# Kernel tuning notes

Measured on AMD Instinct MI355X. Metric: run time of the kernel, lower is better.

Reference implementation:

```python
import jax, jax.numpy as jnp
import numpy as np

E, B, S, D, R = 8, 8, 2048, 512, 128
MAX_MAG = 0.1  # config.geometric.max_rotation_magnitude


def _plane_indices(dim, r):
    # Row-major enumeration of (i, j), i < j, truncated to first r planes,
    # matching the nested loop in create_rotation_matrix.
    pairs = []
    for i in range(dim):
        for j in range(i + 1, dim):
            pairs.append((i, j))
            if len(pairs) == r:
                return np.asarray(pairs, np.int32)
    return np.asarray(pairs, np.int32)


def setup_inputs() -> dict:
    key = jax.random.key(0)
    k1, k2, k3 = jax.random.split(key, 3)
    x = jax.random.normal(k1, (B, S, D), dtype=jnp.float32)
    theta = jax.random.normal(k2, (E, R), dtype=jnp.float32) * 0.1
    # projector init: 0.1 * orthogonal + I  (per torch init in __init__)
    Wr = jax.random.normal(k3, (E, D, D), dtype=jnp.float32)
    Q, _ = jnp.linalg.qr(Wr)
    proj_w = 0.1 * Q + jnp.eye(D, dtype=jnp.float32)
    return {"x": x, "theta": theta, "proj_w": proj_w}


def _rotation_matrix(theta_e, ij):
    # Sequential right-multiplication by Givens rotations.
    # M <- M @ G(i,j,a) only touches columns i and j:
    #   col_i' =  c*col_i + s*col_j ;  col_j' = -s*col_i + c*col_j
    angles = jnp.tanh(theta_e) * MAX_MAG  # [R]

    def step(M, inp):
        i, j, a = inp
        c, s = jnp.cos(a), jnp.sin(a)
        ci = M[:, i]
        cj = M[:, j]
        M = M.at[:, i].set(c * ci + s * cj)
        M = M.at[:, j].set(-s * ci + c * cj)
        return M, None

    M0 = jnp.eye(D, dtype=theta_e.dtype)
    M, _ = jax.lax.scan(step, M0, (ij[:, 0], ij[:, 1], angles))
    return M


def reference(x, theta, proj_w):
    ij = jnp.asarray(_plane_indices(D, R))  # [R, 2] static plane indices
    Rm = jax.vmap(lambda t: _rotation_matrix(t, ij))(theta)  # [E, D, D]
    # rotated = flat_x @ R^T per expert
    rotated = jnp.einsum('bsd,ekd->ebsk', x, Rm)            # [E, B, S, D]
    # projector: Linear(bias=False) -> y = rotated @ W^T
    out = jnp.einsum('ebsk,eok->ebso', rotated, proj_w)     # [E, B, S, D]
    return out
```

## Files before the change

### kernel.cpp

```cpp
#include <hip/hip_runtime.h>
#include <hip/hip_bf16.h>

#define E_ 8
#define B_ 8
#define S_ 2048
#define D_ 512
#define R_ 128
#define M_TOT (B_ * S_)

typedef __attribute__((ext_vector_type(8))) short bf16x8;
typedef __attribute__((ext_vector_type(4))) float f32x4;

__device__ __forceinline__ void gload_lds16(void* lds, const void* g) {
  __builtin_amdgcn_global_load_lds(
      (const __attribute__((address_space(1))) void*)g,
      (__attribute__((address_space(3))) void*)lds, 16, 0, 0);
}

#define ROT_B 16
#define WT_B 2048
#define CX_B 4096
__global__ __launch_bounds__(256) void prep_fused(
    const float* __restrict__ x, const float* __restrict__ theta,
    const float* __restrict__ pw, __hip_bfloat16* __restrict__ xb,
    __hip_bfloat16* __restrict__ Wb) {
  int blk = blockIdx.x;
  int t = threadIdx.x;
  if (blk < ROT_B) {
    __shared__ float cs[R_], ss[R_];
    __shared__ float Pch[256][17];
    __shared__ __hip_bfloat16 Wch[256][18];
    int e = blk >> 1;
    int r0 = (blk & 1) * 256;
    if (t < R_) {
      float a = tanhf(theta[e * R_ + t]) * 0.1f;
      cs[t] = cosf(a);
      ss[t] = sinf(a);
    }
    const float* Pe = pw + (size_t)e * D_ * D_;
    __hip_bfloat16* We = Wb + (size_t)e * D_ * D_;
    float u = Pe[(size_t)(r0 + t) * D_];
    __syncthreads();
    for (int c = 0; c < 8; ++c) {
      for (int i = t; i < 256 * 16; i += 256) {
        int row = i >> 4, col = i & 15;
        Pch[row][col] = Pe[(size_t)(r0 + row) * D_ + 1 + 16 * c + col];
      }
      __syncthreads();
#pragma unroll
      for (int kk = 0; kk < 16; ++kk) {
        int k = 16 * c + kk;
        float pj = Pch[t][kk];
        Wch[t][kk] = __float2bfloat16(cs[k] * pj - ss[k] * u);
        u = cs[k] * u + ss[k] * pj;
      }
      __syncthreads();
      for (int i = t; i < 256 * 16; i += 256) {
        int row = i >> 4, col = i & 15;
        We[(size_t)(r0 + row) * D_ + 1 + 16 * c + col] = Wch[row][col];
      }
      __syncthreads();
    }
    We[(size_t)(r0 + t) * D_] = __float2bfloat16(u);
  } else if (blk < ROT_B + WT_B) {
    int g = (blk - ROT_B) * 256 + t;
    int gidx = g & 127;
    if (gidx < 32) return;
    float4 v = ((const float4*)pw)[g];
    union { short4 s; __hip_bfloat16 h[4]; } u;
    u.h[0] = __float2bfloat16(v.x);
    u.h[1] = __float2bfloat16(v.y);
    u.h[2] = __float2bfloat16(v.z);
    u.h[3] = __float2bfloat16(v.w);
    if (gidx > 32) {
      ((short4*)Wb)[g] = u.s;
    } else {
      Wb[(size_t)g * 4 + 1] = u.h[1];
      Wb[(size_t)g * 4 + 2] = u.h[2];
      Wb[(size_t)g * 4 + 3] = u.h[3];
    }
  } else {
    int i = (blk - ROT_B - WT_B) * 256 + t;
#pragma unroll
    for (int rep = 0; rep < 2; ++rep) {
      int idx = i + rep * (CX_B * 256);
      float4 v = ((const float4*)x)[idx];
      union { short4 s; __hip_bfloat16 h[4]; } u;
      u.h[0] = __float2bfloat16(v.x);
      u.h[1] = __float2bfloat16(v.y);
      u.h[2] = __float2bfloat16(v.z);
      u.h[3] = __float2bfloat16(v.w);
      ((short4*)xb)[idx] = u.s;
    }
  }
}

__global__ __launch_bounds__(512, 2) void gemm_xw(
    const __hip_bfloat16* __restrict__ Xb,
    const __hip_bfloat16* __restrict__ Wb,
    float* __restrict__ out)
{
  constexpr int BK = 64;
  constexpr int KD = D_, ND = D_;
  constexpr int NT = KD / BK;
  __shared__ __align__(16) __hip_bfloat16 As[4][128 * 64];
  __shared__ __align__(16) __hip_bfloat16 Bs[4][128 * 64];

  int bx = blockIdx.x;
  int swz = (bx & 7) * 128 + (bx >> 3);
  int mt = swz >> 4;
  int e  = (swz >> 1) & 7;
  int nt = swz & 1;

  int tid = threadIdx.x;
  int wave = tid >> 6, lane = tid & 63;
  int lr = lane & 15, lk = lane >> 4;
  int wm = wave >> 2, wn = wave & 3;

  const __hip_bfloat16* Ag = Xb + (size_t)(mt * 256) * KD;
  const __hip_bfloat16* Bg = Wb + ((size_t)e * ND + (size_t)nt * 256) * KD;

  int srow = lane >> 3;
  int scol = ((lane & 7) ^ srow) * 8;

  int axor0 = ((0 * 4 + lk) ^ (lr & 7)) * 8;
  int axor1 = ((1 * 4 + lk) ^ (lr & 7)) * 8;

  f32x4 acc[8][4];
#pragma unroll
  for (int i = 0; i < 8; ++i)
#pragma unroll
    for (int j = 0; j < 4; ++j) acc[i][j] = (f32x4){0.f, 0.f, 0.f, 0.f};

#define STAGE(ARR, GBASE, h, tt)                                             \
  {                                                                          \
    int slot_ = (2 * (tt) + (h)) & 3;                                        \
    _Pragma("unroll") for (int g = 0; g < 2; ++g) {                          \
      gload_lds16(&ARR[slot_][(wave * 16 + g * 8) * 64],                     \
                  (GBASE) + (size_t)((h) * 128 + wave * 16 + g * 8 + srow) * \
                                KD + (tt) * BK + scol);                      \
    }                                                                        \
  }

#define QUAD(mh, nh)                                                         \
  {                                                                          \
    __builtin_amdgcn_s_setprio(1);                                           \
    _Pragma("unroll") for (int m4 = 0; m4 < 4; ++m4)                         \
        _Pragma("unroll") for (int n2 = 0; n2 < 2; ++n2)                     \
            _Pragma("unroll") for (int kk = 0; kk < 2; ++kk)                 \
                acc[(mh)*4 + m4][(nh)*2 + n2] =                              \
                    __builtin_amdgcn_mfma_f32_16x16x32_bf16(                 \
                        af[(mh)*4 + m4][kk], bfr[(nh)*2 + n2][kk],           \
                        acc[(mh)*4 + m4][(nh)*2 + n2], 0, 0, 0);             \
    __builtin_amdgcn_s_setprio(0);                                           \
  }

  STAGE(As, Ag, 0, 0); STAGE(As, Ag, 1, 0);
  STAGE(Bs, Bg, 0, 0); STAGE(Bs, Bg, 1, 0);
  STAGE(As, Ag, 0, 1); STAGE(As, Ag, 1, 1);
  STAGE(Bs, Bg, 0, 1);

#pragma unroll
  for (int t = 0; t < NT; ++t) {
    if (t < NT - 1) {
      asm volatile("s_waitcnt vmcnt(6)" ::: "memory");
    } else {
      asm volatile("s_waitcnt vmcnt(0)" ::: "memory");
    }
    __builtin_amdgcn_s_barrier();
    asm volatile("" ::: "memory");

    const __hip_bfloat16* Asl = As[(2 * t + wm) & 3];
    const __hip_bfloat16* Bsl = Bs[(2 * t + (wn >> 1)) & 3];
    bf16x8 af[8][2], bfr[4][2];
#pragma unroll
    for (int mi = 0; mi < 8; ++mi) {
      int rb = (mi * 16 + lr) * 64;
      af[mi][0] = *(const bf16x8*)&Asl[rb + axor0];
      af[mi][1] = *(const bf16x8*)&Asl[rb + axor1];
    }
#pragma unroll
    for (int ni = 0; ni < 4; ++ni) {
      int rb = ((wn & 1) * 64 + ni * 16 + lr) * 64;
      bfr[ni][0] = *(const bf16x8*)&Bsl[rb + axor0];
      bfr[ni][1] = *(const bf16x8*)&Bsl[rb + axor1];
    }
    if (t + 1 < NT) STAGE(Bs, Bg, 1, t + 1);
    __syncthreads();
    QUAD(0, 0);

    if (t + 2 < NT) STAGE(As, Ag, 0, t + 2);
    asm volatile("" ::: "memory");
    __builtin_amdgcn_s_barrier();
    asm volatile("" ::: "memory");
    QUAD(0, 1);

    if (t + 2 < NT) STAGE(As, Ag, 1, t + 2);
    asm volatile("" ::: "memory");
    __builtin_amdgcn_s_barrier();
    asm volatile("" ::: "memory");
    QUAD(1, 0);

    if (t + 2 < NT) STAGE(Bs, Bg, 0, t + 2);
    asm volatile("" ::: "memory");
    __builtin_amdgcn_s_barrier();
    asm volatile("" ::: "memory");
    QUAD(1, 1);
  }
#undef STAGE
#undef QUAD

  size_t obase = (size_t)e * M_TOT * ND;
  int row0 = mt * 256 + wm * 128;
  int col0 = nt * 256 + wn * 64;
#pragma unroll
  for (int mi = 0; mi < 8; ++mi)
#pragma unroll
    for (int ni = 0; ni < 4; ++ni) {
      int r0 = row0 + mi * 16 + lk * 4;
      int c = col0 + ni * 16 + lr;
      float* op = out + obase + (size_t)r0 * ND + c;
#pragma unroll
      for (int q = 0; q < 4; ++q) op[(size_t)q * ND] = acc[mi][ni][q];
    }
}

extern "C" void kernel_launch(void* const* d_in, const int* in_sizes, int n_in,
                              void* d_out, int out_size, void* d_ws, size_t ws_size,
                              hipStream_t stream) {
  const float* x = (const float*)d_in[0];
  const float* theta = (const float*)d_in[1];
  const float* proj_w = (const float*)d_in[2];
  float* out = (float*)d_out;

  __hip_bfloat16* xb = (__hip_bfloat16*)d_ws;
  __hip_bfloat16* Wb = (__hip_bfloat16*)((char*)d_ws +
                        (size_t)M_TOT * D_ * sizeof(__hip_bfloat16));

  hipLaunchKernelGGL(prep_fused, dim3(ROT_B + WT_B + CX_B), dim3(256), 0,
                     stream, x, theta, proj_w, xb, Wb);
  hipLaunchKernelGGL(gemm_xw, dim3(E_ * (M_TOT / 256) * (D_ / 256)), dim3(512),
                     0, stream, xb, Wb, out);
}
```

Before: 128.1 us.

## Split LDS fragment loads into phases interleaved with MFMA quadrants

The GEMM main loop now loads A and B fragments from shared memory in halves, just before the MFMA quadrant that needs them, instead of loading all fragments up front. Explicit lgkmcnt waits and sched barriers enforce the order. The global-to-LDS prefetch order is also rearranged so slots are refilled only after every wave has finished reading them. The aim is to overlap LDS reads with matrix work and to lower peak fragment register pressure. The cost is extra barriers and waits, which could serialize the waves.

```diff
diff --git a/kernel.cpp b/kernel.cpp
--- a/kernel.cpp
+++ b/kernel.cpp
@@ -142,7 +142,7 @@
     }                                                                        \
   }
 
-#define QUAD(mh, nh)                                                         \
+#define QUAD(AF, BF, mh, nh)                                                 \
   {                                                                          \
     __builtin_amdgcn_s_setprio(1);                                           \
     _Pragma("unroll") for (int m4 = 0; m4 < 4; ++m4)                         \
@@ -150,15 +150,19 @@
             _Pragma("unroll") for (int kk = 0; kk < 2; ++kk)                 \
                 acc[(mh)*4 + m4][(nh)*2 + n2] =                              \
                     __builtin_amdgcn_mfma_f32_16x16x32_bf16(                 \
-                        af[(mh)*4 + m4][kk], bfr[(nh)*2 + n2][kk],           \
+                        AF[m4][kk], BF[n2][kk],                              \
                         acc[(mh)*4 + m4][(nh)*2 + n2], 0, 0, 0);             \
     __builtin_amdgcn_s_setprio(0);                                           \
   }
 
+#define LGKM0                                                                \
+  asm volatile("s_waitcnt lgkmcnt(0)" ::: "memory");                         \
+  __builtin_amdgcn_sched_barrier(0);
+
   STAGE(As, Ag, 0, 0); STAGE(As, Ag, 1, 0);
   STAGE(Bs, Bg, 0, 0); STAGE(Bs, Bg, 1, 0);
+  STAGE(Bs, Bg, 0, 1);
   STAGE(As, Ag, 0, 1); STAGE(As, Ag, 1, 1);
-  STAGE(Bs, Bg, 0, 1);
 
 #pragma unroll
   for (int t = 0; t < NT; ++t) {
@@ -168,47 +172,58 @@
       asm volatile("s_waitcnt vmcnt(0)" ::: "memory");
     }
     __builtin_amdgcn_s_barrier();
-    asm volatile("" ::: "memory");
 
     const __hip_bfloat16* Asl = As[(2 * t + wm) & 3];
     const __hip_bfloat16* Bsl = Bs[(2 * t + (wn >> 1)) & 3];
-    bf16x8 af[8][2], bfr[4][2];
-#pragma unroll
-    for (int mi = 0; mi < 8; ++mi) {
+
+    bf16x8 af_lo[4][2], bfr_lo[2][2];
+#pragma unroll
+    for (int mi = 0; mi < 4; ++mi) {
       int rb = (mi * 16 + lr) * 64;
-      af[mi][0] = *(const bf16x8*)&Asl[rb + axor0];
-      af[mi][1] = *(const bf16x8*)&Asl[rb + axor1];
-    }
-#pragma unroll
-    for (int ni = 0; ni < 4; ++ni) {
+      af_lo[mi][0] = *(const bf16x8*)&Asl[rb + axor0];
+      af_lo[mi][1] = *(const bf16x8*)&Asl[rb + axor1];
+    }
+#pragma unroll
+    for (int ni = 0; ni < 2; ++ni) {
       int rb = ((wn & 1) * 64 + ni * 16 + lr) * 64;
-      bfr[ni][0] = *(const bf16x8*)&Bsl[rb + axor0];
-      bfr[ni][1] = *(const bf16x8*)&Bsl[rb + axor1];
+      bfr_lo[ni][0] = *(const bf16x8*)&Bsl[rb + axor0];
+      bfr_lo[ni][1] = *(const bf16x8*)&Bsl[rb + axor1];
     }
     if (t + 1 < NT) STAGE(Bs, Bg, 1, t + 1);
-    __syncthreads();
-    QUAD(0, 0);
-
-    if (t + 2 < NT) STAGE(As, Ag, 0, t + 2);
-    asm volatile("" ::: "memory");
-    __builtin_amdgcn_s_barrier();
-    asm volatile("" ::: "memory");
-    QUAD(0, 1);
-
-    if (t + 2 < NT) STAGE(As, Ag, 1, t + 2);
-    asm volatile("" ::: "memory");
-    __builtin_amdgcn_s_barrier();
-    asm volatile("" ::: "memory");
-    QUAD(1, 0);
-
+    LGKM0;
+    __builtin_amdgcn_s_barrier();
+    QUAD(af_lo, bfr_lo, 0, 0);
+
+    bf16x8 bfr_hi[2][2];
+#pragma unroll
+    for (int ni = 0; ni < 2; ++ni) {
+      int rb = ((wn & 1) * 64 + (2 + ni) * 16 + lr) * 64;
+      bfr_hi[ni][0] = *(const bf16x8*)&Bsl[rb + axor0];
+      bfr_hi[ni][1] = *(const bf16x8*)&Bsl[rb + axor1];
+    }
+    LGKM0;
+    __builtin_amdgcn_s_barrier();
+    QUAD(af_lo, bfr_hi, 0, 1);
+
+    bf16x8 af_hi[4][2];
+#pragma unroll
+    for (int mi = 0; mi < 4; ++mi) {
+      int rb = ((4 + mi) * 16 + lr) * 64;
+      af_hi[mi][0] = *(const bf16x8*)&Asl[rb + axor0];
+      af_hi[mi][1] = *(const bf16x8*)&Asl[rb + axor1];
+    }
     if (t + 2 < NT) STAGE(Bs, Bg, 0, t + 2);
-    asm volatile("" ::: "memory");
-    __builtin_amdgcn_s_barrier();
-    asm volatile("" ::: "memory");
-    QUAD(1, 1);
+    LGKM0;
+    __builtin_amdgcn_s_barrier();
+    QUAD(af_hi, bfr_lo, 1, 0);
+
+    if (t + 2 < NT) { STAGE(As, Ag, 0, t + 2); STAGE(As, Ag, 1, t + 2); }
+    __builtin_amdgcn_s_barrier();
+    QUAD(af_hi, bfr_hi, 1, 1);
   }
 #undef STAGE
 #undef QUAD
+#undef LGKM0
 
   size_t obase = (size_t)e * M_TOT * ND;
   int row0 = mt * 256 + wm * 128;
```

Measured after the change: 129.0 us. About the same (+0.8%).
